# Kernel tuning notes

Measured on AMD Instinct MI355X. Metric: run time of the kernel, lower is better.

## Reference

```python
import jax, jax.numpy as jnp
import numpy as np

N = 100000          # nodes
E = 1000000         # edges (before self loops)
F_IN = 128          # node feature dim
HEADS = [4, 2, 2]   # gat_heads
D = 48              # per-head out channels (hardcoded in module)
G = 64              # number of graphs in batch
FC_DIM = 192
OUT_DIM = 96
NEG_SLOPE = 0.2     # PyG GATConv default


def setup_inputs() -> dict:
    key = jax.random.key(0)
    ks = jax.random.split(key, 32)
    d = {
        "x": jax.random.normal(ks[0], (N, F_IN), jnp.float32),
        "edge_index": jax.random.randint(ks[1], (2, E), 0, N, dtype=jnp.int64),
        "batch": jnp.sort(jax.random.randint(ks[2], (N,), 0, G, dtype=jnp.int64)),
    }
    in_ch = F_IN
    k = 3
    for i, h in enumerate(HEADS):
        d[f"W{i}"] = jax.random.normal(ks[k], (in_ch, h * D), jnp.float32) / np.sqrt(in_ch); k += 1
        d[f"att_src{i}"] = jax.random.normal(ks[k], (h, D), jnp.float32) * 0.1; k += 1
        d[f"att_dst{i}"] = jax.random.normal(ks[k], (h, D), jnp.float32) * 0.1; k += 1
        d[f"bias{i}"] = jnp.zeros((h * D,), jnp.float32)
        in_ch = h * D
    d["fcW1"] = jax.random.normal(ks[k], (in_ch, FC_DIM), jnp.float32) / np.sqrt(in_ch); k += 1
    d["fcb1"] = jnp.zeros((FC_DIM,), jnp.float32)
    d["fcW2"] = jax.random.normal(ks[k], (FC_DIM, OUT_DIM), jnp.float32) / np.sqrt(FC_DIM); k += 1
    d["fcb2"] = jnp.zeros((OUT_DIM,), jnp.float32)
    return d


def _gat_layer(x, W, att_src, att_dst, bias, src, dst, heads):
    n = x.shape[0]
    h = (x @ W).reshape(n, heads, D)                    # [N,H,D]
    a_src = jnp.sum(h * att_src, axis=-1)               # [N,H]
    a_dst = jnp.sum(h * att_dst, axis=-1)               # [N,H]
    e = jax.nn.leaky_relu(a_src[src] + a_dst[dst], NEG_SLOPE)   # [Et,H]
    # segment softmax over incoming edges at each destination node
    m = jax.ops.segment_max(e, dst, num_segments=n)
    e = jnp.exp(e - m[dst])
    denom = jax.ops.segment_sum(e, dst, num_segments=n)
    alpha = e / (denom[dst] + 1e-16)                    # [Et,H]
    msg = h[src] * alpha[..., None]                     # [Et,H,D]
    out = jax.ops.segment_sum(msg, dst, num_segments=n) # [N,H,D]
    return out.reshape(n, heads * D) + bias


def reference(x, edge_index, batch,
              W0, att_src0, att_dst0, bias0,
              W1, att_src1, att_dst1, bias1,
              W2, att_src2, att_dst2, bias2,
              fcW1, fcb1, fcW2, fcb2):
    n = x.shape[0]
    loops = jnp.arange(n, dtype=edge_index.dtype)
    src = jnp.concatenate([edge_index[0], loops])   # add self loops (PyG default)
    dst = jnp.concatenate([edge_index[1], loops])
    x = jax.nn.relu(_gat_layer(x, W0, att_src0, att_dst0, bias0, src, dst, HEADS[0]))
    x = jax.nn.relu(_gat_layer(x, W1, att_src1, att_dst1, bias1, src, dst, HEADS[1]))
    x = jax.nn.relu(_gat_layer(x, W2, att_src2, att_dst2, bias2, src, dst, HEADS[2]))
    # global mean pool over graphs
    sums = jax.ops.segment_sum(x, batch, num_segments=G)
    counts = jax.ops.segment_sum(jnp.ones((n, 1), x.dtype), batch, num_segments=G)
    pooled = sums / jnp.maximum(counts, 1.0)
    h = jax.nn.relu(pooled @ fcW1 + fcb1)
    return h @ fcW2 + fcb2
```

## Files before the change

kernel.cpp:

```cpp
#include <hip/hip_runtime.h>

#define CAP 64
#define DD 48

typedef short v8s __attribute__((ext_vector_type(8)));
typedef float v4f __attribute__((ext_vector_type(4)));
typedef float v2f __attribute__((ext_vector_type(2)));

__device__ __forceinline__ unsigned int bf16r(float f) {
    unsigned int u = __float_as_uint(f);
    return (u + 0x7FFFu + ((u >> 16) & 1u)) >> 16;
}

__device__ __forceinline__ v8s ld_frag(const ushort* p) {
    const uint2* q = reinterpret_cast<const uint2*>(p);
    uint2 a = q[0], b = q[1];
    union { unsigned int u[4]; v8s v; } t;
    t.u[0] = a.x; t.u[1] = a.y; t.u[2] = b.x; t.u[3] = b.y;
    return t.v;
}

__global__ void build_adj_kernel(const int* __restrict__ ei, int E, int N,
                                 int* __restrict__ cnt, int* __restrict__ adj) {
    int e = blockIdx.x * blockDim.x + threadIdx.x;
    int Et = E + N;
    if (e >= Et) return;
    int s, d;
    if (e < E) { s = ei[e]; d = ei[E + e]; } else { s = e - E; d = e - E; }
    int pos = atomicAdd(&cnt[d], 1);
    if (pos < CAP) adj[d * CAP + pos] = s;
}

__global__ void cast_x_kernel(const float* __restrict__ x, unsigned int* __restrict__ xb, long n2) {
    long i = (long)blockIdx.x * blockDim.x + threadIdx.x;
    if (i >= n2) return;
    float2 v = reinterpret_cast<const float2*>(x)[i];
    xb[i] = bf16r(v.x) | (bf16r(v.y) << 16);
}

__global__ void convw_kernel(const float* __restrict__ W, ushort* __restrict__ WT, int K, int NC) {
    int i = blockIdx.x * blockDim.x + threadIdx.x;
    if (i >= K * NC) return;
    int k = i / NC, n = i % NC;
    WT[n * K + k] = (ushort)bf16r(W[i]);
}

template<int K, int NCT, int HEADS>
__global__ void gemm_mfma(const ushort* __restrict__ Xb, const ushort* __restrict__ WT,
                          const float* __restrict__ att_s, const float* __restrict__ att_d,
                          ushort* __restrict__ Hb, float* __restrict__ asrc,
                          float* __restrict__ adst, int N) {
    __shared__ ushort XT_l[128 * 40];
    __shared__ ushort WT_l[96 * 40];
    int tid = threadIdx.x;
    int wv = tid >> 6, lane = tid & 63;
    int m = lane & 15, quad = lane >> 4;
    int rb = blockIdx.x * 128;
    int c0 = blockIdx.y * 96;
    int mw = wv * 32;
    v4f acc[2][6];
#pragma unroll
    for (int mi = 0; mi < 2; mi++)
#pragma unroll
        for (int nb = 0; nb < 6; nb++) acc[mi][nb] = (v4f){0.f, 0.f, 0.f, 0.f};

    for (int k0 = 0; k0 < K; k0 += 32) {
#pragma unroll
        for (int t = 0; t < 2; t++) {
            int ch = tid + t * 256;
            int r = ch >> 2, kq = ch & 3;
            int rg = rb + r;
            uint4 v = make_uint4(0u, 0u, 0u, 0u);
            if (rg < N) v = *reinterpret_cast<const uint4*>(&Xb[(long)rg * K + k0 + kq * 8]);
            uint2* d = reinterpret_cast<uint2*>(&XT_l[r * 40 + kq * 8]);
            d[0] = make_uint2(v.x, v.y);
            d[1] = make_uint2(v.z, v.w);
        }
#pragma unroll
        for (int t = 0; t < 2; t++) {
            int ch = tid + t * 256;
            if (ch < 384) {
                int wr = ch >> 2, kq = ch & 3;
                uint4 v = *reinterpret_cast<const uint4*>(&WT[(long)(c0 + wr) * K + k0 + kq * 8]);
                uint2* d = reinterpret_cast<uint2*>(&WT_l[wr * 40 + kq * 8]);
                d[0] = make_uint2(v.x, v.y);
                d[1] = make_uint2(v.z, v.w);
            }
        }
        __syncthreads();
        v8s af[2], bf[6];
        af[0] = ld_frag(&XT_l[(mw + m) * 40 + quad * 8]);
        af[1] = ld_frag(&XT_l[(mw + 16 + m) * 40 + quad * 8]);
#pragma unroll
        for (int nb = 0; nb < 6; nb++)
            bf[nb] = ld_frag(&WT_l[(nb * 16 + m) * 40 + quad * 8]);
#pragma unroll
        for (int mi = 0; mi < 2; mi++)
#pragma unroll
            for (int nb = 0; nb < 6; nb++)
                acc[mi][nb] = __builtin_amdgcn_mfma_f32_16x16x32_bf16(af[mi], bf[nb], acc[mi][nb], 0, 0, 0);
        __syncthreads();
    }

#pragma unroll
    for (int mi = 0; mi < 2; mi++)
#pragma unroll
        for (int r = 0; r < 4; r++) {
            int R = rb + mw + mi * 16 + quad * 4 + r;
            if (R < N) {
#pragma unroll
                for (int nb = 0; nb < 6; nb++)
                    Hb[(long)R * NCT + c0 + nb * 16 + m] = (ushort)bf16r(acc[mi][nb][r]);
            }
        }

    float aS[6], aD[6];
    int h0 = c0 / DD;
#pragma unroll
    for (int nb = 0; nb < 6; nb++) {
        int cb = nb * 16 + m;
        int hl = cb / DD;
        int cih = cb - hl * DD;
        aS[nb] = att_s[(h0 + hl) * DD + cih];
        aD[nb] = att_d[(h0 + hl) * DD + cih];
    }
#pragma unroll
    for (int mi = 0; mi < 2; mi++)
#pragma unroll
        for (int r = 0; r < 4; r++) {
            float ps0 = 0.f, ps1 = 0.f, pd0 = 0.f, pd1 = 0.f;
#pragma unroll
            for (int nb = 0; nb < 3; nb++) {
                ps0 = fmaf(acc[mi][nb][r], aS[nb], ps0);
                pd0 = fmaf(acc[mi][nb][r], aD[nb], pd0);
            }
#pragma unroll
            for (int nb = 3; nb < 6; nb++) {
                ps1 = fmaf(acc[mi][nb][r], aS[nb], ps1);
                pd1 = fmaf(acc[mi][nb][r], aD[nb], pd1);
            }
#pragma unroll
            for (int d = 1; d < 16; d <<= 1) {
                ps0 += __shfl_xor(ps0, d); ps1 += __shfl_xor(ps1, d);
                pd0 += __shfl_xor(pd0, d); pd1 += __shfl_xor(pd1, d);
            }
            int R = rb + mw + mi * 16 + quad * 4 + r;
            if (m == 0 && R < N) {
                asrc[R * HEADS + h0]     = ps0;
                asrc[R * HEADS + h0 + 1] = ps1;
                adst[R * HEADS + h0]     = pd0;
                adst[R * HEADS + h0 + 1] = pd1;
            }
        }
}

template<int OUT, int HEADS, int PAIRS, bool OBF16>
__global__ void agg_kernel(const unsigned int* __restrict__ Hb,
                           const float* __restrict__ asrc, const float* __restrict__ adst,
                           const int* __restrict__ adj, const int* __restrict__ cnt,
                           const float* __restrict__ bias,
                           unsigned int* __restrict__ Ob, float* __restrict__ Of, int N) {
    typedef unsigned int pk_t __attribute__((ext_vector_type(PAIRS)));
    constexpr int NL = OUT / (2 * PAIRS);
    __shared__ float wlds[4][HEADS][CAP + 1];
    __shared__ float dlds[4][HEADS];
    __shared__ int   slds[4][CAP];
    int wv = threadIdx.x >> 6;
    int lane = threadIdx.x & 63;
    int n = blockIdx.x * 4 + wv;
    bool valid = (n < N);
    int nn = valid ? n : 0;
    int deg_raw = cnt[nn];
    int araw = adj[nn * CAP + lane];
    int deg = min(deg_raw, CAP);
    int s = (lane < deg) ? araw : 0;
    slds[wv][lane] = s;

    float av[HEADS];
    if constexpr (HEADS == 4) {
        float4 t = *reinterpret_cast<const float4*>(&asrc[s * 4]);
        av[0] = t.x; av[1] = t.y; av[2] = t.z; av[3] = t.w;
    } else {
        float2 t = *reinterpret_cast<const float2*>(&asrc[s * 2]);
        av[0] = t.x; av[1] = t.y;
    }
    float w[HEADS];
#pragma unroll
    for (int h = 0; h < HEADS; h++) {
        float e = av[h] + adst[nn * HEADS + h];
        e = (e < 0.f) ? 0.2f * e : e;
        w[h] = (lane < deg) ? __expf(e) : 0.f;
        wlds[wv][h][lane] = w[h];
    }
#pragma unroll
    for (int h = 0; h < HEADS; h++) {
        float dsum = w[h];
#pragma unroll
        for (int off = 1; off < 64; off <<= 1) dsum += __shfl_xor(dsum, off);
        if (lane == 0) dlds[wv][h] = dsum;
    }
    __syncthreads();

    bool act = (lane < NL);
    int c = act ? lane * 2 * PAIRS : 0;
    int head = c / DD;
    const float* wrow = &wlds[wv][head][0];
    v2f acc2[PAIRS];
#pragma unroll
    for (int q = 0; q < PAIRS; q++) acc2[q] = (v2f){0.f, 0.f};

    for (int i = 0; i < deg; i += 4) {
        int sv[4];
#pragma unroll
        for (int u = 0; u < 4; u++) sv[u] = slds[wv][i + u];
        pk_t hv[4];
#pragma unroll
        for (int u = 0; u < 4; u++)
            hv[u] = *reinterpret_cast<const pk_t*>(&Hb[((long)sv[u] * OUT + c) >> 1]);
#pragma unroll
        for (int u = 0; u < 4; u++) {
            float ww = wrow[i + u];
#pragma unroll
            for (int q = 0; q < PAIRS; q++) {
                v2f h2;
                h2.x = __uint_as_float(hv[u][q] << 16);
                h2.y = __uint_as_float(hv[u][q] & 0xFFFF0000u);
                acc2[q] += ww * h2;
            }
        }
    }

    if (valid && act) {
        float invd = 1.f / (dlds[wv][head] + 1e-16f);
        if (OBF16) {
            pk_t pk;
#pragma unroll
            for (int q = 0; q < PAIRS; q++) {
                float o0 = fmaxf(fmaf(acc2[q].x, invd, bias[c + 2 * q]), 0.f);
                float o1 = fmaxf(fmaf(acc2[q].y, invd, bias[c + 2 * q + 1]), 0.f);
                pk[q] = bf16r(o0) | (bf16r(o1) << 16);
            }
            *reinterpret_cast<pk_t*>(&Ob[((long)n * OUT + c) >> 1]) = pk;
        } else {
#pragma unroll
            for (int q = 0; q < PAIRS; q++) {
                float o0 = fmaxf(fmaf(acc2[q].x, invd, bias[c + 2 * q]), 0.f);
                float o1 = fmaxf(fmaf(acc2[q].y, invd, bias[c + 2 * q + 1]), 0.f);
                *reinterpret_cast<float2*>(&Of[(long)n * OUT + c + 2 * q]) = make_float2(o0, o1);
            }
        }
    }
}

__global__ void pool_kernel(const float* __restrict__ O, const int* __restrict__ batch,
                            float* __restrict__ sums, float* __restrict__ counts, int N) {
    int grp = threadIdx.x >> 7;
    int c = threadIdx.x & 127;
    int n0 = (blockIdx.x * 4 + grp) * 64;
    if (n0 >= N) return;
    int nend = min(N, n0 + 64);
    bool act = (c < 96);
    float acc = 0.f; int cl = 0;
    int cur = batch[n0];
    int n = n0;
    for (; n + 4 <= nend; n += 4) {
        int g0 = batch[n], g1 = batch[n + 1], g2 = batch[n + 2], g3 = batch[n + 3];
        float v0 = 0.f, v1 = 0.f, v2 = 0.f, v3 = 0.f;
        if (act) {
            v0 = O[(long)n * 96 + c];       v1 = O[(long)(n + 1) * 96 + c];
            v2 = O[(long)(n + 2) * 96 + c]; v3 = O[(long)(n + 3) * 96 + c];
        }
#define POOL_STEP(g, v)                                                        \
        if ((g) != cur) {                                                      \
            if (act) atomicAdd(&sums[cur * 96 + c], acc);                      \
            if (c == 96) atomicAdd(&counts[cur], (float)cl);                   \
            acc = 0.f; cl = 0; cur = (g);                                      \
        }                                                                      \
        acc += (v); cl++;
        POOL_STEP(g0, v0) POOL_STEP(g1, v1) POOL_STEP(g2, v2) POOL_STEP(g3, v3)
    }
    for (; n < nend; n++) {
        int g = batch[n];
        float v = act ? O[(long)n * 96 + c] : 0.f;
        POOL_STEP(g, v)
    }
#undef POOL_STEP
    if (act) atomicAdd(&sums[cur * 96 + c], acc);
    if (c == 96) atomicAdd(&counts[cur], (float)cl);
}

__global__ void fc_kernel(const float* __restrict__ sums, const float* __restrict__ counts,
                          const float* __restrict__ W1, const float* __restrict__ b1,
                          const float* __restrict__ W2, const float* __restrict__ b2,
                          float* __restrict__ out) {
    __shared__ float p[96];
    __shared__ float h1[192];
    int g = blockIdx.x, tid = threadIdx.x;
    if (tid < 96) p[tid] = sums[g * 96 + tid] / fmaxf(counts[g], 1.0f);
    __syncthreads();
    float s = b1[tid];
    for (int c = 0; c < 96; c++) s = fmaf(p[c], W1[c * 192 + tid], s);
    h1[tid] = fmaxf(s, 0.f);
    __syncthreads();
    if (tid < 96) {
        float s2 = b2[tid];
        for (int j = 0; j < 192; j++) s2 = fmaf(h1[j], W2[j * 96 + tid], s2);
        out[g * 96 + tid] = s2;
    }
}

extern "C" void kernel_launch(void* const* d_in, const int* in_sizes, int n_in,
                              void* d_out, int out_size, void* d_ws, size_t ws_size,
                              hipStream_t stream) {
    const float* x     = (const float*)d_in[0];
    const int*   ei    = (const int*)d_in[1];
    const int*   batch = (const int*)d_in[2];
    const float* W0  = (const float*)d_in[3];
    const float* as0 = (const float*)d_in[4];
    const float* ad0 = (const float*)d_in[5];
    const float* b0  = (const float*)d_in[6];
    const float* W1  = (const float*)d_in[7];
    const float* as1 = (const float*)d_in[8];
    const float* ad1 = (const float*)d_in[9];
    const float* b1  = (const float*)d_in[10];
    const float* W2  = (const float*)d_in[11];
    const float* as2 = (const float*)d_in[12];
    const float* ad2 = (const float*)d_in[13];
    const float* b2  = (const float*)d_in[14];
    const float* fcW1 = (const float*)d_in[15];
    const float* fcb1 = (const float*)d_in[16];
    const float* fcW2 = (const float*)d_in[17];
    const float* fcb2 = (const float*)d_in[18];

    const int N = in_sizes[0] / 128;
    const int E = in_sizes[1] / 2;

    char* ws = (char*)d_ws;
    unsigned int* Xb   = (unsigned int*)ws;
    unsigned int* Hb   = (unsigned int*)(ws + (size_t)N * 256);
    unsigned int* Ob   = (unsigned int*)(ws + (size_t)N * 640);
    float*        Obuf = (float*)(ws + (size_t)N * 1024);
    float*        ASRC = (float*)(ws + (size_t)N * 1408);
    float*        ADST = (float*)(ws + (size_t)N * 1424);
    int*          ADJ  = (int*)(ws + (size_t)N * 1440);
    int*          CNT  = (int*)(ws + (size_t)N * 1696);
    float*        SUMS = (float*)(ws + (size_t)N * 1700);
    float*        COUNTS = SUMS + 64 * 96;
    ushort*       WT0  = (ushort*)(COUNTS + 64);
    ushort*       WT1  = WT0 + 192 * 128;
    ushort*       WT2  = WT1 + 96 * 192;

    hipMemsetAsync(CNT, 0, (size_t)N * 4 + (64 * 96 + 64) * 4, stream);

    int Et = E + N;
    build_adj_kernel<<<(Et + 255) / 256, 256, 0, stream>>>(ei, E, N, CNT, ADJ);

    long n2 = (long)N * 64;
    cast_x_kernel<<<(int)((n2 + 255) / 256), 256, 0, stream>>>(x, Xb, n2);
    convw_kernel<<<(128 * 192 + 255) / 256, 256, 0, stream>>>(W0, WT0, 128, 192);
    convw_kernel<<<(192 * 96 + 255) / 256, 256, 0, stream>>>(W1, WT1, 192, 96);
    convw_kernel<<<(96 * 96 + 255) / 256, 256, 0, stream>>>(W2, WT2, 96, 96);

    int gb = (N + 127) / 128;

    gemm_mfma<128, 192, 4><<<dim3(gb, 2), 256, 0, stream>>>((const ushort*)Xb, WT0, as0, ad0,
                                                            (ushort*)Hb, ASRC, ADST, N);
    agg_kernel<192, 4, 2, true><<<(N + 3) / 4, 256, 0, stream>>>(Hb, ASRC, ADST, ADJ, CNT, b0, Ob, nullptr, N);

    gemm_mfma<192, 96, 2><<<dim3(gb, 1), 256, 0, stream>>>((const ushort*)Ob, WT1, as1, ad1,
                                                           (ushort*)Hb, ASRC, ADST, N);
    agg_kernel<96, 2, 1, true><<<(N + 3) / 4, 256, 0, stream>>>(Hb, ASRC, ADST, ADJ, CNT, b1, Ob, nullptr, N);

    gemm_mfma<96, 96, 2><<<dim3(gb, 1), 256, 0, stream>>>((const ushort*)Ob, WT2, as2, ad2,
                                                          (ushort*)Hb, ASRC, ADST, N);
    agg_kernel<96, 2, 1, false><<<(N + 3) / 4, 256, 0, stream>>>(Hb, ASRC, ADST, ADJ, CNT, b2, nullptr, Obuf, N);

    pool_kernel<<<(N / 256) + 1, 512, 0, stream>>>(Obuf, batch, SUMS, COUNTS, N);
    fc_kernel<<<64, 192, 0, stream>>>(SUMS, COUNTS, fcW1, fcb1, fcW2, fcb2, (float*)d_out);
}
```

Baseline: 493.7 us.

## Split wave across four edges per step in GAT aggregation with cross-lane reduction

The aggregation kernel now assigns 16-lane sub-groups to different edges, so each wave gathers four neighbor rows at once in 32-channel slices, instead of each lane covering a fixed channel range and walking all edges serially. Partial sums are then reduced across sub-groups with shuffles before normalization, bias and ReLU. For the 96-wide layers this keeps all 64 lanes busy where previously only 48 were, and it should increase memory-level parallelism for the irregular gathers. The cost is narrower 4-byte loads per lane, extra shuffle reductions, and per-slice head selection logic. The adst values are also loaded as one vector instead of separate scalars.

```diff
diff --git a/kernel.cpp b/kernel.cpp
--- a/kernel.cpp
+++ b/kernel.cpp
@@ -154,19 +154,21 @@
         }
 }
 
-template<int OUT, int HEADS, int PAIRS, bool OBF16>
+template<int OUT, int HEADS, bool OBF16>
 __global__ void agg_kernel(const unsigned int* __restrict__ Hb,
                            const float* __restrict__ asrc, const float* __restrict__ adst,
                            const int* __restrict__ adj, const int* __restrict__ cnt,
                            const float* __restrict__ bias,
                            unsigned int* __restrict__ Ob, float* __restrict__ Of, int N) {
-    typedef unsigned int pk_t __attribute__((ext_vector_type(PAIRS)));
-    constexpr int NL = OUT / (2 * PAIRS);
+    constexpr int SLICES = OUT / 32;
+    constexpr int ROWU = OUT / 2;
     __shared__ float wlds[4][HEADS][CAP + 1];
     __shared__ float dlds[4][HEADS];
     __shared__ int   slds[4][CAP];
     int wv = threadIdx.x >> 6;
     int lane = threadIdx.x & 63;
+    int esub = lane >> 4;
+    int lp   = lane & 15;
     int n = blockIdx.x * 4 + wv;
     bool valid = (n < N);
     int nn = valid ? n : 0;
@@ -176,18 +178,22 @@
     int s = (lane < deg) ? araw : 0;
     slds[wv][lane] = s;
 
-    float av[HEADS];
+    float av[HEADS], dvv[HEADS];
     if constexpr (HEADS == 4) {
         float4 t = *reinterpret_cast<const float4*>(&asrc[s * 4]);
         av[0] = t.x; av[1] = t.y; av[2] = t.z; av[3] = t.w;
+        float4 u = *reinterpret_cast<const float4*>(&adst[nn * 4]);
+        dvv[0] = u.x; dvv[1] = u.y; dvv[2] = u.z; dvv[3] = u.w;
     } else {
         float2 t = *reinterpret_cast<const float2*>(&asrc[s * 2]);
         av[0] = t.x; av[1] = t.y;
+        float2 u = *reinterpret_cast<const float2*>(&adst[nn * 2]);
+        dvv[0] = u.x; dvv[1] = u.y;
     }
     float w[HEADS];
 #pragma unroll
     for (int h = 0; h < HEADS; h++) {
-        float e = av[h] + adst[nn * HEADS + h];
+        float e = av[h] + dvv[h];
         e = (e < 0.f) ? 0.2f * e : e;
         w[h] = (lane < deg) ? __expf(e) : 0.f;
         wlds[wv][h][lane] = w[h];
@@ -201,53 +207,67 @@
     }
     __syncthreads();
 
-    bool act = (lane < NL);
-    int c = act ? lane * 2 * PAIRS : 0;
-    int head = c / DD;
-    const float* wrow = &wlds[wv][head][0];
-    v2f acc2[PAIRS];
-#pragma unroll
-    for (int q = 0; q < PAIRS; q++) acc2[q] = (v2f){0.f, 0.f};
-
-    for (int i = 0; i < deg; i += 4) {
-        int sv[4];
-#pragma unroll
-        for (int u = 0; u < 4; u++) sv[u] = slds[wv][i + u];
-        pk_t hv[4];
-#pragma unroll
-        for (int u = 0; u < 4; u++)
-            hv[u] = *reinterpret_cast<const pk_t*>(&Hb[((long)sv[u] * OUT + c) >> 1]);
-#pragma unroll
-        for (int u = 0; u < 4; u++) {
-            float ww = wrow[i + u];
-#pragma unroll
-            for (int q = 0; q < PAIRS; q++) {
+    v2f acc2[SLICES];
+#pragma unroll
+    for (int sl = 0; sl < SLICES; sl++) acc2[sl] = (v2f){0.f, 0.f};
+
+    for (int base = 0; base < deg; base += 16) {
+        int se[4];
+        float we[HEADS][4];
+#pragma unroll
+        for (int g = 0; g < 4; g++) {
+            int e = base + (g << 2) + esub;
+            se[g] = slds[wv][e];
+#pragma unroll
+            for (int h = 0; h < HEADS; h++) we[h][g] = wlds[wv][h][e];
+        }
+#pragma unroll
+        for (int sl = 0; sl < SLICES; sl++) {
+            unsigned int hv[4];
+#pragma unroll
+            for (int g = 0; g < 4; g++)
+                hv[g] = Hb[se[g] * ROWU + sl * 16 + lp];
+            constexpr int hA0 = 0;  (void)hA0;
+#pragma unroll
+            for (int g = 0; g < 4; g++) {
+                int hA = (sl * 32) / DD;
+                int hB = (sl * 32 + 30) / DD;
+                float ww;
+                if (hA == hB) ww = we[hA][g];
+                else {
+                    int cut = (hB * DD - sl * 32) >> 1;
+                    ww = (lp < cut) ? we[hA][g] : we[hB][g];
+                }
                 v2f h2;
-                h2.x = __uint_as_float(hv[u][q] << 16);
-                h2.y = __uint_as_float(hv[u][q] & 0xFFFF0000u);
-                acc2[q] += ww * h2;
-            }
-        }
-    }
-
-    if (valid && act) {
-        float invd = 1.f / (dlds[wv][head] + 1e-16f);
-        if (OBF16) {
-            pk_t pk;
-#pragma unroll
-            for (int q = 0; q < PAIRS; q++) {
-                float o0 = fmaxf(fmaf(acc2[q].x, invd, bias[c + 2 * q]), 0.f);
-                float o1 = fmaxf(fmaf(acc2[q].y, invd, bias[c + 2 * q + 1]), 0.f);
-                pk[q] = bf16r(o0) | (bf16r(o1) << 16);
-            }
-            *reinterpret_cast<pk_t*>(&Ob[((long)n * OUT + c) >> 1]) = pk;
-        } else {
-#pragma unroll
-            for (int q = 0; q < PAIRS; q++) {
-                float o0 = fmaxf(fmaf(acc2[q].x, invd, bias[c + 2 * q]), 0.f);
-                float o1 = fmaxf(fmaf(acc2[q].y, invd, bias[c + 2 * q + 1]), 0.f);
-                *reinterpret_cast<float2*>(&Of[(long)n * OUT + c + 2 * q]) = make_float2(o0, o1);
-            }
+                h2.x = __uint_as_float(hv[g] << 16);
+                h2.y = __uint_as_float(hv[g] & 0xFFFF0000u);
+                acc2[sl] += ww * h2;
+            }
+        }
+    }
+
+#pragma unroll
+    for (int sl = 0; sl < SLICES; sl++) {
+        float ax = acc2[sl].x, ay = acc2[sl].y;
+        ax += __shfl_xor(ax, 16); ay += __shfl_xor(ay, 16);
+        ax += __shfl_xor(ax, 32); ay += __shfl_xor(ay, 32);
+        if (valid && esub == 0) {
+            int hA = (sl * 32) / DD;
+            int hB = (sl * 32 + 30) / DD;
+            float den;
+            if (hA == hB) den = dlds[wv][hA];
+            else {
+                int cut = (hB * DD - sl * 32) >> 1;
+                den = (lp < cut) ? dlds[wv][hA] : dlds[wv][hB];
+            }
+            float invd = 1.f / (den + 1e-16f);
+            int ch = sl * 32 + lp * 2;
+            float o0 = fmaxf(fmaf(ax, invd, bias[ch]), 0.f);
+            float o1 = fmaxf(fmaf(ay, invd, bias[ch + 1]), 0.f);
+            if (OBF16)
+                Ob[((long)n * OUT + ch) >> 1] = bf16r(o0) | (bf16r(o1) << 16);
+            else
+                *reinterpret_cast<float2*>(&Of[(long)n * OUT + ch]) = make_float2(o0, o1);
         }
     }
 }
@@ -365,15 +385,15 @@
 
     gemm_mfma<128, 192, 4><<<dim3(gb, 2), 256, 0, stream>>>((const ushort*)Xb, WT0, as0, ad0,
                                                             (ushort*)Hb, ASRC, ADST, N);
-    agg_kernel<192, 4, 2, true><<<(N + 3) / 4, 256, 0, stream>>>(Hb, ASRC, ADST, ADJ, CNT, b0, Ob, nullptr, N);
+    agg_kernel<192, 4, true><<<(N + 3) / 4, 256, 0, stream>>>(Hb, ASRC, ADST, ADJ, CNT, b0, Ob, nullptr, N);
 
     gemm_mfma<192, 96, 2><<<dim3(gb, 1), 256, 0, stream>>>((const ushort*)Ob, WT1, as1, ad1,
                                                            (ushort*)Hb, ASRC, ADST, N);
-    agg_kernel<96, 2, 1, true><<<(N + 3) / 4, 256, 0, stream>>>(Hb, ASRC, ADST, ADJ, CNT, b1, Ob, nullptr, N);
+    agg_kernel<96, 2, true><<<(N + 3) / 4, 256, 0, stream>>>(Hb, ASRC, ADST, ADJ, CNT, b1, Ob, nullptr, N);
 
     gemm_mfma<96, 96, 2><<<dim3(gb, 1), 256, 0, stream>>>((const ushort*)Ob, WT2, as2, ad2,
                                                           (ushort*)Hb, ASRC, ADST, N);
-    agg_kernel<96, 2, 1, false><<<(N + 3) / 4, 256, 0, stream>>>(Hb, ASRC, ADST, ADJ, CNT, b2, nullptr, Obuf, N);
+    agg_kernel<96, 2, false><<<(N + 3) / 4, 256, 0, stream>>>(Hb, ASRC, ADST, ADJ, CNT, b2, nullptr, Obuf, N);
 
     pool_kernel<<<(N / 256) + 1, 512, 0, stream>>>(Obuf, batch, SUMS, COUNTS, N);
     fc_kernel<<<64, 192, 0, stream>>>(SUMS, COUNTS, fcW1, fcb1, fcW2, fcb2, (float*)d_out);
```

After: 519.7 us. 5.3% more time.

## Split aggregation lanes across edges to use the full wavefront

Applied to the files above, without the earlier changes.

The GAT aggregation kernel now gives each lane a 6-column slice and spreads the wavefront's lanes over several edges at once: 2 edges per step for the 192-wide layer and 4 for the 96-wide layers. Partial sums are then combined with cross-lane shuffles. Previously only 48 of 64 lanes were active and each lane walked every edge serially. The goal is better lane utilisation and more gather loads in flight, at the cost of shuffle reductions, odd-sized uint3 loads, and some wasted work on padded edges. The adst values are also read with one vector load instead of scalar loads.

```diff
diff --git a/kernel.cpp b/kernel.cpp
--- a/kernel.cpp
+++ b/kernel.cpp
@@ -154,19 +154,21 @@
         }
 }
 
-template<int OUT, int HEADS, int PAIRS, bool OBF16>
+template<int OUT, int HEADS, int EPW, bool OBF16>
 __global__ void agg_kernel(const unsigned int* __restrict__ Hb,
                            const float* __restrict__ asrc, const float* __restrict__ adst,
                            const int* __restrict__ adj, const int* __restrict__ cnt,
                            const float* __restrict__ bias,
                            unsigned int* __restrict__ Ob, float* __restrict__ Of, int N) {
-    typedef unsigned int pk_t __attribute__((ext_vector_type(PAIRS)));
-    constexpr int NL = OUT / (2 * PAIRS);
+    constexpr int LPE = 64 / EPW;
+    constexpr int ROWU = OUT / 2;
     __shared__ float wlds[4][HEADS][CAP + 1];
     __shared__ float dlds[4][HEADS];
     __shared__ int   slds[4][CAP];
     int wv = threadIdx.x >> 6;
     int lane = threadIdx.x & 63;
+    int esub = lane / LPE;
+    int lp   = lane % LPE;
     int n = blockIdx.x * 4 + wv;
     bool valid = (n < N);
     int nn = valid ? n : 0;
@@ -176,18 +178,22 @@
     int s = (lane < deg) ? araw : 0;
     slds[wv][lane] = s;
 
-    float av[HEADS];
+    float av[HEADS], dvv[HEADS];
     if constexpr (HEADS == 4) {
         float4 t = *reinterpret_cast<const float4*>(&asrc[s * 4]);
         av[0] = t.x; av[1] = t.y; av[2] = t.z; av[3] = t.w;
+        float4 u = *reinterpret_cast<const float4*>(&adst[nn * 4]);
+        dvv[0] = u.x; dvv[1] = u.y; dvv[2] = u.z; dvv[3] = u.w;
     } else {
         float2 t = *reinterpret_cast<const float2*>(&asrc[s * 2]);
         av[0] = t.x; av[1] = t.y;
+        float2 u = *reinterpret_cast<const float2*>(&adst[nn * 2]);
+        dvv[0] = u.x; dvv[1] = u.y;
     }
     float w[HEADS];
 #pragma unroll
     for (int h = 0; h < HEADS; h++) {
-        float e = av[h] + adst[nn * HEADS + h];
+        float e = av[h] + dvv[h];
         e = (e < 0.f) ? 0.2f * e : e;
         w[h] = (lane < deg) ? __expf(e) : 0.f;
         wlds[wv][h][lane] = w[h];
@@ -201,53 +207,59 @@
     }
     __syncthreads();
 
-    bool act = (lane < NL);
-    int c = act ? lane * 2 * PAIRS : 0;
+    int c = lp * 6;
     int head = c / DD;
     const float* wrow = &wlds[wv][head][0];
-    v2f acc2[PAIRS];
-#pragma unroll
-    for (int q = 0; q < PAIRS; q++) acc2[q] = (v2f){0.f, 0.f};
-
-    for (int i = 0; i < deg; i += 4) {
-        int sv[4];
-#pragma unroll
-        for (int u = 0; u < 4; u++) sv[u] = slds[wv][i + u];
-        pk_t hv[4];
-#pragma unroll
-        for (int u = 0; u < 4; u++)
-            hv[u] = *reinterpret_cast<const pk_t*>(&Hb[((long)sv[u] * OUT + c) >> 1]);
-#pragma unroll
-        for (int u = 0; u < 4; u++) {
-            float ww = wrow[i + u];
-#pragma unroll
-            for (int q = 0; q < PAIRS; q++) {
-                v2f h2;
-                h2.x = __uint_as_float(hv[u][q] << 16);
-                h2.y = __uint_as_float(hv[u][q] & 0xFFFF0000u);
-                acc2[q] += ww * h2;
-            }
-        }
-    }
-
-    if (valid && act) {
+    v2f a0 = (v2f){0.f, 0.f}, a1 = (v2f){0.f, 0.f}, a2 = (v2f){0.f, 0.f};
+
+    for (int base = 0; base < deg; base += 2 * EPW) {
+        int e0 = base + esub, e1 = base + EPW + esub;
+        int s0 = slds[wv][e0], s1 = slds[wv][e1];
+        uint3 h0 = *reinterpret_cast<const uint3*>(&Hb[(long)s0 * ROWU + lp * 3]);
+        uint3 h1 = *reinterpret_cast<const uint3*>(&Hb[(long)s1 * ROWU + lp * 3]);
+        float w0 = wrow[e0], w1 = wrow[e1];
+        v2f p;
+        p.x = __uint_as_float(h0.x << 16); p.y = __uint_as_float(h0.x & 0xFFFF0000u);
+        a0 += w0 * p;
+        p.x = __uint_as_float(h0.y << 16); p.y = __uint_as_float(h0.y & 0xFFFF0000u);
+        a1 += w0 * p;
+        p.x = __uint_as_float(h0.z << 16); p.y = __uint_as_float(h0.z & 0xFFFF0000u);
+        a2 += w0 * p;
+        p.x = __uint_as_float(h1.x << 16); p.y = __uint_as_float(h1.x & 0xFFFF0000u);
+        a0 += w1 * p;
+        p.x = __uint_as_float(h1.y << 16); p.y = __uint_as_float(h1.y & 0xFFFF0000u);
+        a1 += w1 * p;
+        p.x = __uint_as_float(h1.z << 16); p.y = __uint_as_float(h1.z & 0xFFFF0000u);
+        a2 += w1 * p;
+    }
+
+#pragma unroll
+    for (int off = LPE; off < 64; off <<= 1) {
+        a0.x += __shfl_xor(a0.x, off); a0.y += __shfl_xor(a0.y, off);
+        a1.x += __shfl_xor(a1.x, off); a1.y += __shfl_xor(a1.y, off);
+        a2.x += __shfl_xor(a2.x, off); a2.y += __shfl_xor(a2.y, off);
+    }
+
+    if (valid && esub == 0) {
         float invd = 1.f / (dlds[wv][head] + 1e-16f);
+        float o[6];
+        o[0] = fmaxf(fmaf(a0.x, invd, bias[c + 0]), 0.f);
+        o[1] = fmaxf(fmaf(a0.y, invd, bias[c + 1]), 0.f);
+        o[2] = fmaxf(fmaf(a1.x, invd, bias[c + 2]), 0.f);
+        o[3] = fmaxf(fmaf(a1.y, invd, bias[c + 3]), 0.f);
+        o[4] = fmaxf(fmaf(a2.x, invd, bias[c + 4]), 0.f);
+        o[5] = fmaxf(fmaf(a2.y, invd, bias[c + 5]), 0.f);
         if (OBF16) {
-            pk_t pk;
-#pragma unroll
-            for (int q = 0; q < PAIRS; q++) {
-                float o0 = fmaxf(fmaf(acc2[q].x, invd, bias[c + 2 * q]), 0.f);
-                float o1 = fmaxf(fmaf(acc2[q].y, invd, bias[c + 2 * q + 1]), 0.f);
-                pk[q] = bf16r(o0) | (bf16r(o1) << 16);
-            }
-            *reinterpret_cast<pk_t*>(&Ob[((long)n * OUT + c) >> 1]) = pk;
+            uint3 pk;
+            pk.x = bf16r(o[0]) | (bf16r(o[1]) << 16);
+            pk.y = bf16r(o[2]) | (bf16r(o[3]) << 16);
+            pk.z = bf16r(o[4]) | (bf16r(o[5]) << 16);
+            *reinterpret_cast<uint3*>(&Ob[(long)n * ROWU + lp * 3]) = pk;
         } else {
-#pragma unroll
-            for (int q = 0; q < PAIRS; q++) {
-                float o0 = fmaxf(fmaf(acc2[q].x, invd, bias[c + 2 * q]), 0.f);
-                float o1 = fmaxf(fmaf(acc2[q].y, invd, bias[c + 2 * q + 1]), 0.f);
-                *reinterpret_cast<float2*>(&Of[(long)n * OUT + c + 2 * q]) = make_float2(o0, o1);
-            }
+            float* dst = &Of[(long)n * OUT + c];
+            *reinterpret_cast<float2*>(dst)     = make_float2(o[0], o[1]);
+            *reinterpret_cast<float2*>(dst + 2) = make_float2(o[2], o[3]);
+            *reinterpret_cast<float2*>(dst + 4) = make_float2(o[4], o[5]);
         }
     }
 }
@@ -369,11 +381,11 @@
 
     gemm_mfma<192, 96, 2><<<dim3(gb, 1), 256, 0, stream>>>((const ushort*)Ob, WT1, as1, ad1,
                                                            (ushort*)Hb, ASRC, ADST, N);
-    agg_kernel<96, 2, 1, true><<<(N + 3) / 4, 256, 0, stream>>>(Hb, ASRC, ADST, ADJ, CNT, b1, Ob, nullptr, N);
+    agg_kernel<96, 2, 4, true><<<(N + 3) / 4, 256, 0, stream>>>(Hb, ASRC, ADST, ADJ, CNT, b1, Ob, nullptr, N);
 
     gemm_mfma<96, 96, 2><<<dim3(gb, 1), 256, 0, stream>>>((const ushort*)Ob, WT2, as2, ad2,
                                                           (ushort*)Hb, ASRC, ADST, N);
-    agg_kernel<96, 2, 1, false><<<(N + 3) / 4, 256, 0, stream>>>(Hb, ASRC, ADST, ADJ, CNT, b2, nullptr, Obuf, N);
+    agg_kernel<96, 2, 4, false><<<(N + 3) / 4, 256, 0, stream>>>(Hb, ASRC, ADST, ADJ, CNT, b2, nullptr, Obuf, N);
 
     pool_kernel<<<(N / 256) + 1, 512, 0, stream>>>(Obuf, batch, SUMS, COUNTS, N);
     fc_kernel<<<64, 192, 0, stream>>>(SUMS, COUNTS, fcW1, fcb1, fcW2, fcb2, (float*)d_out);
```

After: 480.4 us. -2.7%, faster.
